# Kernel tuning notes

Hardware: AMD Instinct MI355X
Metric: run time of the kernel (lower is better)

The kernel has to match this reference:

```python
import jax, jax.numpy as jnp
import numpy as np

NUM_HEADS = 8
EPS = 1e-6


def setup_inputs() -> dict:
    key = jax.random.key(0)
    k1, k2, k3 = jax.random.split(key, 3)
    B, N, C = 4, 256, 512
    x = jax.random.normal(k1, (B, N, C), dtype=jnp.float32)
    w_qkv = jax.random.normal(k2, (3 * C, C), dtype=jnp.float32) * (C ** -0.5)
    w_proj = jax.random.normal(k3, (C, C), dtype=jnp.float32) * (C ** -0.5)
    b_proj = jnp.zeros((C,), dtype=jnp.float32)
    paramR = jnp.ones((1,), dtype=jnp.float32)
    return {"x": x, "w_qkv": w_qkv, "w_proj": w_proj, "b_proj": b_proj, "paramR": paramR}


def _fourier_attention(x, w_qkv, w_proj, b_proj, paramR):
    B, N, C = x.shape
    H = NUM_HEADS
    Dh = C // H
    # qkv projection (no bias), split into per-head q,k,v: (B,H,N,Dh)
    qkv = jnp.einsum('bnc,kc->bnk', x, w_qkv).reshape(B, N, 3, H, Dh)
    q = qkv[:, :, 0].transpose(0, 2, 1, 3)
    k = qkv[:, :, 1].transpose(0, 2, 1, 3)
    v = qkv[:, :, 2].transpose(0, 2, 1, 3)
    R = paramR[0]
    # Generalized Fourier integral kernel: prod_d sin(R*(q_d - k_d))/(q_d - k_d)
    diff = q[:, :, :, None, :] - k[:, :, None, :, :]  # (B,H,Nq,Nk,Dh)
    near0 = jnp.abs(diff) < 1e-8
    safe = jnp.where(near0, jnp.float32(1.0), diff)
    s = jnp.where(near0, R, jnp.sin(R * safe) / safe)
    score = jnp.prod(s, axis=-1)  # (B,H,Nq,Nk)
    a4 = score ** 4
    attn = a4 / (jnp.sum(a4, axis=-1, keepdims=True) + EPS)  # normalize over keys
    out = jnp.einsum('bhqk,bhkd->bhqd', attn, v)
    out = out.transpose(0, 2, 1, 3).reshape(B, N, C)
    return jnp.einsum('bnc,oc->bno', out, w_proj) + b_proj


def reference(x, w_qkv, w_proj, b_proj, paramR):
    return _fourier_attention(x, w_qkv, w_proj, b_proj, paramR)
```

## Files before the change

kernel.cpp:

```cpp
#include <hip/hip_runtime.h>
#include <math.h>

#define BB 4
#define NN 256
#define CC 512
#define HH 8
#define DH 64

typedef __attribute__((ext_vector_type(8))) short bf16x8;
typedef __attribute__((ext_vector_type(4))) float f32x4;

__device__ inline unsigned short f2bf(float f) {
  unsigned u = __float_as_uint(f);
  u += 0x7FFFu + ((u >> 16) & 1u);
  return (unsigned short)(u >> 16);
}
__device__ inline float bf2f(unsigned short s) {
  return __uint_as_float((unsigned)s << 16);
}

__global__ __launch_bounds__(256) void cvt_hilo3(
    const float* __restrict__ in0, unsigned short* __restrict__ h0,
    unsigned short* __restrict__ l0, const float* __restrict__ in1,
    unsigned short* __restrict__ h1, unsigned short* __restrict__ l1,
    const float* __restrict__ in2, unsigned short* __restrict__ h2,
    unsigned short* __restrict__ l2) {
  int b = blockIdx.x;
  const float* in;
  unsigned short *h, *l;
  if (b < 512) {
    in = in0; h = h0; l = l0;
  } else if (b < 1280) {
    in = in1; h = h1; l = l1; b -= 512;
  } else {
    in = in2; h = h2; l = l2; b -= 1280;
  }
  int i = (b * 256 + threadIdx.x) * 4;
  float4 f = *(const float4*)(in + i);
  float fa[4] = {f.x, f.y, f.z, f.w};
  ushort4 hv, lv;
  unsigned short* hp = (unsigned short*)&hv;
  unsigned short* lp = (unsigned short*)&lv;
#pragma unroll
  for (int j = 0; j < 4; j++) {
    unsigned short hb = f2bf(fa[j]);
    hp[j] = hb;
    lp[j] = f2bf(fa[j] - bf2f(hb));
  }
  *(ushort4*)(h + i) = hv;
  *(ushort4*)(l + i) = lv;
}

template <bool BIAS>
__global__ __launch_bounds__(256, 2) void gemm_mfma(
    const unsigned short* __restrict__ Ah, const unsigned short* __restrict__ Al,
    const unsigned short* __restrict__ Bh, const unsigned short* __restrict__ Bl,
    const float* __restrict__ bias, float* __restrict__ C, int M, int N,
    int K) {
  __shared__ unsigned short sAh[64][72], sAl[64][72];
  __shared__ unsigned short sBh[64][72], sBl[64][72];
  const int t = threadIdx.x;
  const int lane = t & 63;
  const int w = t >> 6;
  const int bm = blockIdx.y * 64;
  const int bn = blockIdx.x * 64;
  const int wr = (w >> 1) * 32;
  const int wc = (w & 1) * 32;
  const int quad = lane >> 4;
  const int l16 = lane & 15;

  const int r0 = t >> 3;
  const int r1 = r0 + 32;
  const int c8 = (t & 7) * 8;

  const size_t a0 = (size_t)(bm + r0) * K + c8;
  const size_t a1 = (size_t)(bm + r1) * K + c8;
  const size_t b0 = (size_t)(bn + r0) * K + c8;
  const size_t b1 = (size_t)(bn + r1) * K + c8;

  f32x4 acc[2][2];
#pragma unroll
  for (int i = 0; i < 2; i++)
#pragma unroll
    for (int j = 0; j < 2; j++) {
      acc[i][j][0] = 0.f;
      acc[i][j][1] = 0.f;
      acc[i][j][2] = 0.f;
      acc[i][j][3] = 0.f;
    }

  uint4 pa0, pa1, pa2, pa3, pb0, pb1, pb2, pb3;
#define GLOADS(K0)                          \
  pa0 = *(const uint4*)(Ah + a0 + (K0));    \
  pa1 = *(const uint4*)(Ah + a1 + (K0));    \
  pa2 = *(const uint4*)(Al + a0 + (K0));    \
  pa3 = *(const uint4*)(Al + a1 + (K0));    \
  pb0 = *(const uint4*)(Bh + b0 + (K0));    \
  pb1 = *(const uint4*)(Bh + b1 + (K0));    \
  pb2 = *(const uint4*)(Bl + b0 + (K0));    \
  pb3 = *(const uint4*)(Bl + b1 + (K0));

  GLOADS(0)

  for (int k0 = 0; k0 < K; k0 += 64) {
    __syncthreads();
    *(uint4*)&sAh[r0][c8] = pa0;
    *(uint4*)&sAh[r1][c8] = pa1;
    *(uint4*)&sAl[r0][c8] = pa2;
    *(uint4*)&sAl[r1][c8] = pa3;
    *(uint4*)&sBh[r0][c8] = pb0;
    *(uint4*)&sBh[r1][c8] = pb1;
    *(uint4*)&sBl[r0][c8] = pb2;
    *(uint4*)&sBl[r1][c8] = pb3;
    __syncthreads();
    if (k0 + 64 < K) {
      GLOADS(k0 + 64)
    }
#pragma unroll
    for (int kk = 0; kk < 2; kk++) {
      const int kc = kk * 32 + quad * 8;
      bf16x8 ah[2], al[2], bh[2], bl[2];
#pragma unroll
      for (int i = 0; i < 2; i++) {
        ah[i] = *(const bf16x8*)&sAh[wr + i * 16 + l16][kc];
        al[i] = *(const bf16x8*)&sAl[wr + i * 16 + l16][kc];
        bh[i] = *(const bf16x8*)&sBh[wc + i * 16 + l16][kc];
        bl[i] = *(const bf16x8*)&sBl[wc + i * 16 + l16][kc];
      }
#pragma unroll
      for (int i = 0; i < 2; i++)
#pragma unroll
        for (int j = 0; j < 2; j++) {
          acc[i][j] = __builtin_amdgcn_mfma_f32_16x16x32_bf16(
              ah[i], bh[j], acc[i][j], 0, 0, 0);
          acc[i][j] = __builtin_amdgcn_mfma_f32_16x16x32_bf16(
              ah[i], bl[j], acc[i][j], 0, 0, 0);
          acc[i][j] = __builtin_amdgcn_mfma_f32_16x16x32_bf16(
              al[i], bh[j], acc[i][j], 0, 0, 0);
        }
    }
  }
#undef GLOADS

#pragma unroll
  for (int i = 0; i < 2; i++)
#pragma unroll
    for (int j = 0; j < 2; j++) {
      int n = bn + wc + j * 16 + l16;
      float bv = BIAS ? bias[n] : 0.f;
#pragma unroll
      for (int r = 0; r < 4; r++) {
        int m = bm + wr + i * 16 + quad * 4 + r;
        C[(size_t)m * N + n] = acc[i][j][r] + bv;
      }
    }
}

__global__ __launch_bounds__(512, 4) void fourier_attn(
    const float* __restrict__ qkv, const float* __restrict__ paramR,
    unsigned short* __restrict__ aoh, unsigned short* __restrict__ aol) {
  __shared__ float Kt[64][68];
  __shared__ float VtT[64][68];
  __shared__ float Qs[16][DH];
  __shared__ float A4[8][64][2];

  const int t = threadIdx.x;
  const int lane = t & 63;
  const int wv = t >> 6;
  const int qc = blockIdx.x;
  const int h = blockIdx.y;
  const int b = blockIdx.z;
  const float R = paramR[0];
  const float cR = R * 0.15915494309189535f;

  const float* base = qkv + (size_t)b * NN * (3 * CC) + h * DH;

  if (t < 256) {
    int r = t >> 4;
    int c4 = (t & 15) << 2;
    *(float4*)&Qs[r][c4] =
        *(const float4*)(base + (size_t)(qc * 16 + r) * (3 * CC) + c4);
  }

  const int qi0 = wv * 2, qi1 = wv * 2 + 1;
  float Sp[2] = {0.f, 0.f};
  float acc[2] = {0.f, 0.f};

  float4 pk[2], pv[2];
#define LOADT(JT)                                                   \
  _Pragma("unroll") for (int u0 = 0; u0 < 2; u0++) {                \
    int u = t + 512 * u0;                                           \
    int r_ = u >> 4;                                                \
    int c4_ = (u & 15) << 2;                                        \
    const float* row_ = base + (size_t)((JT) * 64 + r_) * (3 * CC); \
    pk[u0] = *(const float4*)(row_ + CC + c4_);                     \
    pv[u0] = *(const float4*)(row_ + 2 * CC + c4_);                 \
  }

  LOADT(0)

  for (int jt = 0; jt < 4; jt++) {
    __syncthreads();
#pragma unroll
    for (int u0 = 0; u0 < 2; u0++) {
      int u = t + 512 * u0;
      int r = u >> 4;
      int c4 = (u & 15) << 2;
      *(float4*)&Kt[r][c4] = pk[u0];
      int rs = r ^ c4;
      float4 vv = pv[u0];
      VtT[c4 + 0][rs] = vv.x;
      VtT[c4 + 1][rs] = vv.y;
      VtT[c4 + 2][rs] = vv.z;
      VtT[c4 + 3][rs] = vv.w;
    }
    __syncthreads();
    if (jt < 3) {
      LOADT(jt + 1)
    }

    float nm[2][2] = {{1.f, 1.f}, {1.f, 1.f}};
    float dn[2][2] = {{1.f, 1.f}, {1.f, 1.f}};
#pragma unroll
    for (int d4 = 0; d4 < 16; d4++) {
      const int p = d4 & 1;
      float4 k4 = *(const float4*)&Kt[lane][4 * d4];
      float4 qa = *(const float4*)&Qs[qi0][4 * d4];
      float4 qb = *(const float4*)&Qs[qi1][4 * d4];
      float ka[4] = {k4.x, k4.y, k4.z, k4.w};
      float q0a[4] = {qa.x, qa.y, qa.z, qa.w};
      float q1a[4] = {qb.x, qb.y, qb.z, qb.w};
#pragma unroll
      for (int j = 0; j < 4; j++) {
        float d0 = q0a[j] - ka[j] + 1e-30f;
        float d1 = q1a[j] - ka[j] + 1e-30f;
        nm[0][p] *= __builtin_amdgcn_sinf(cR * d0);
        dn[0][p] *= d0;
        nm[1][p] *= __builtin_amdgcn_sinf(cR * d1);
        dn[1][p] *= d1;
      }
    }
#pragma unroll
    for (int q = 0; q < 2; q++) {
      float sc = (nm[q][0] * nm[q][1]) / (dn[q][0] * dn[q][1]);
      float s2 = sc * sc;
      float a4 = s2 * s2;
      Sp[q] += a4;
      A4[wv][lane][q] = a4;
    }

#pragma unroll
    for (int j4 = 0; j4 < 16; j4++) {
      float4 v4 = *(const float4*)&VtT[lane][(4 * j4) ^ (lane & 60)];
      float4 a01 = *(const float4*)&A4[wv][4 * j4 + 0][0];
      float4 a23 = *(const float4*)&A4[wv][4 * j4 + 2][0];
      acc[0] = fmaf(a01.x, v4.x, acc[0]);
      acc[1] = fmaf(a01.y, v4.x, acc[1]);
      acc[0] = fmaf(a01.z, v4.y, acc[0]);
      acc[1] = fmaf(a01.w, v4.y, acc[1]);
      acc[0] = fmaf(a23.x, v4.z, acc[0]);
      acc[1] = fmaf(a23.y, v4.z, acc[1]);
      acc[0] = fmaf(a23.z, v4.w, acc[0]);
      acc[1] = fmaf(a23.w, v4.w, acc[1]);
    }
  }
#undef LOADT

#pragma unroll
  for (int q = 0; q < 2; q++) {
    float s = Sp[q];
#pragma unroll
    for (int off = 32; off > 0; off >>= 1) s += __shfl_xor(s, off, 64);
    float o = acc[q] / (s + 1e-6f);
    int n = qc * 16 + wv * 2 + q;
    size_t idx = (size_t)(b * NN + n) * CC + h * DH + lane;
    unsigned short oh = f2bf(o);
    aoh[idx] = oh;
    aol[idx] = f2bf(o - bf2f(oh));
  }
}

extern "C" void kernel_launch(void* const* d_in, const int* in_sizes, int n_in,
                              void* d_out, int out_size, void* d_ws,
                              size_t ws_size, hipStream_t stream) {
  const float* x = (const float*)d_in[0];
  const float* w_qkv = (const float*)d_in[1];
  const float* w_proj = (const float*)d_in[2];
  const float* b_proj = (const float*)d_in[3];
  const float* paramR = (const float*)d_in[4];
  float* outp = (float*)d_out;

  const int nX = BB * NN * CC;
  const int nWq = 3 * CC * CC;
  const int nWp = CC * CC;

  unsigned short* xh = (unsigned short*)d_ws;
  unsigned short* xl = xh + nX;
  unsigned short* wqh = xl + nX;
  unsigned short* wql = wqh + nWq;
  unsigned short* wph = wql + nWq;
  unsigned short* wpl = wph + nWp;
  unsigned short* aoh = wpl + nWp;
  unsigned short* aol = aoh + nX;
  float* qkv_ws = (float*)(aol + nX);

  cvt_hilo3<<<1536, 256, 0, stream>>>(x, xh, xl, w_qkv, wqh, wql, w_proj, wph,
                                      wpl);

  gemm_mfma<false><<<dim3(3 * CC / 64, BB * NN / 64), 256, 0, stream>>>(
      xh, xl, wqh, wql, nullptr, qkv_ws, BB * NN, 3 * CC, CC);

  fourier_attn<<<dim3(NN / 16, HH, BB), 512, 0, stream>>>(qkv_ws, paramR, aoh,
                                                          aol);

  gemm_mfma<true><<<dim3(CC / 64, BB * NN / 64), 256, 0, stream>>>(
      aoh, aol, wph, wpl, b_proj, outp, BB * NN, CC, CC);
}
```

Before: 123.0 us.

## Use MFMA for attention PV product and double-buffer GEMM shared tiles

The scalar FMA loop for attention weights times V becomes split-bf16 (hi/lo) MFMA operations. The weights are staged in shared memory as bf16 hi/lo pairs, and the 8 waves split the key range into two halves that are reduced at the end. The GEMM kernel gains double-buffered LDS tiles, which removes one barrier per K step. The sine/product loop is also rewritten with 2-wide float vectors to encourage packed math. The cost is an extra barrier per key tile, the split-bf16 conversion overhead, and more LDS use in the GEMM.

```diff
diff --git a/kernel.cpp b/kernel.cpp
--- a/kernel.cpp
+++ b/kernel.cpp
@@ -9,6 +9,7 @@
 
 typedef __attribute__((ext_vector_type(8))) short bf16x8;
 typedef __attribute__((ext_vector_type(4))) float f32x4;
+typedef __attribute__((ext_vector_type(2))) float f32x2;
 
 __device__ inline unsigned short f2bf(float f) {
   unsigned u = __float_as_uint(f);
@@ -57,8 +58,8 @@
     const unsigned short* __restrict__ Bh, const unsigned short* __restrict__ Bl,
     const float* __restrict__ bias, float* __restrict__ C, int M, int N,
     int K) {
-  __shared__ unsigned short sAh[64][72], sAl[64][72];
-  __shared__ unsigned short sBh[64][72], sBl[64][72];
+  __shared__ unsigned short sAh[2][64][72], sAl[2][64][72];
+  __shared__ unsigned short sBh[2][64][72], sBl[2][64][72];
   const int t = threadIdx.x;
   const int lane = t & 63;
   const int w = t >> 6;
@@ -90,42 +91,43 @@
     }
 
   uint4 pa0, pa1, pa2, pa3, pb0, pb1, pb2, pb3;
-#define GLOADS(K0)                          \
-  pa0 = *(const uint4*)(Ah + a0 + (K0));    \
-  pa1 = *(const uint4*)(Ah + a1 + (K0));    \
-  pa2 = *(const uint4*)(Al + a0 + (K0));    \
-  pa3 = *(const uint4*)(Al + a1 + (K0));    \
-  pb0 = *(const uint4*)(Bh + b0 + (K0));    \
-  pb1 = *(const uint4*)(Bh + b1 + (K0));    \
-  pb2 = *(const uint4*)(Bl + b0 + (K0));    \
+#define GLOADS(K0)                       \
+  pa0 = *(const uint4*)(Ah + a0 + (K0)); \
+  pa1 = *(const uint4*)(Ah + a1 + (K0)); \
+  pa2 = *(const uint4*)(Al + a0 + (K0)); \
+  pa3 = *(const uint4*)(Al + a1 + (K0)); \
+  pb0 = *(const uint4*)(Bh + b0 + (K0)); \
+  pb1 = *(const uint4*)(Bh + b1 + (K0)); \
+  pb2 = *(const uint4*)(Bl + b0 + (K0)); \
   pb3 = *(const uint4*)(Bl + b1 + (K0));
 
+#define STORE(P)                  \
+  *(uint4*)&sAh[P][r0][c8] = pa0; \
+  *(uint4*)&sAh[P][r1][c8] = pa1; \
+  *(uint4*)&sAl[P][r0][c8] = pa2; \
+  *(uint4*)&sAl[P][r1][c8] = pa3; \
+  *(uint4*)&sBh[P][r0][c8] = pb0; \
+  *(uint4*)&sBh[P][r1][c8] = pb1; \
+  *(uint4*)&sBl[P][r0][c8] = pb2; \
+  *(uint4*)&sBl[P][r1][c8] = pb3;
+
   GLOADS(0)
-
+  STORE(0)
+  __syncthreads();
+  GLOADS(64)
+
+  int p = 0;
   for (int k0 = 0; k0 < K; k0 += 64) {
-    __syncthreads();
-    *(uint4*)&sAh[r0][c8] = pa0;
-    *(uint4*)&sAh[r1][c8] = pa1;
-    *(uint4*)&sAl[r0][c8] = pa2;
-    *(uint4*)&sAl[r1][c8] = pa3;
-    *(uint4*)&sBh[r0][c8] = pb0;
-    *(uint4*)&sBh[r1][c8] = pb1;
-    *(uint4*)&sBl[r0][c8] = pb2;
-    *(uint4*)&sBl[r1][c8] = pb3;
-    __syncthreads();
-    if (k0 + 64 < K) {
-      GLOADS(k0 + 64)
-    }
 #pragma unroll
     for (int kk = 0; kk < 2; kk++) {
       const int kc = kk * 32 + quad * 8;
       bf16x8 ah[2], al[2], bh[2], bl[2];
 #pragma unroll
       for (int i = 0; i < 2; i++) {
-        ah[i] = *(const bf16x8*)&sAh[wr + i * 16 + l16][kc];
-        al[i] = *(const bf16x8*)&sAl[wr + i * 16 + l16][kc];
-        bh[i] = *(const bf16x8*)&sBh[wc + i * 16 + l16][kc];
-        bl[i] = *(const bf16x8*)&sBl[wc + i * 16 + l16][kc];
+        ah[i] = *(const bf16x8*)&sAh[p][wr + i * 16 + l16][kc];
+        al[i] = *(const bf16x8*)&sAl[p][wr + i * 16 + l16][kc];
+        bh[i] = *(const bf16x8*)&sBh[p][wc + i * 16 + l16][kc];
+        bl[i] = *(const bf16x8*)&sBl[p][wc + i * 16 + l16][kc];
       }
 #pragma unroll
       for (int i = 0; i < 2; i++)
@@ -139,8 +141,17 @@
               al[i], bh[j], acc[i][j], 0, 0, 0);
         }
     }
+    if (k0 + 64 < K) {
+      STORE(p ^ 1)
+      if (k0 + 128 < K) {
+        GLOADS(k0 + 128)
+      }
+    }
+    __syncthreads();
+    p ^= 1;
   }
 #undef GLOADS
+#undef STORE
 
 #pragma unroll
   for (int i = 0; i < 2; i++)
@@ -160,13 +171,18 @@
     const float* __restrict__ qkv, const float* __restrict__ paramR,
     unsigned short* __restrict__ aoh, unsigned short* __restrict__ aol) {
   __shared__ float Kt[64][68];
-  __shared__ float VtT[64][68];
-  __shared__ float Qs[16][DH];
-  __shared__ float A4[8][64][2];
+  __shared__ float Vs[64][68];
+  __shared__ float Qs[16][64];
+  __shared__ unsigned short Pah[16][72];
+  __shared__ unsigned short Pal[16][72];
+  __shared__ float Sden[16];
+  __shared__ f32x4 Red[4][64];
 
   const int t = threadIdx.x;
   const int lane = t & 63;
   const int wv = t >> 6;
+  const int quad = lane >> 4;
+  const int l16 = lane & 15;
   const int qc = blockIdx.x;
   const int h = blockIdx.y;
   const int b = blockIdx.z;
@@ -184,7 +200,12 @@
 
   const int qi0 = wv * 2, qi1 = wv * 2 + 1;
   float Sp[2] = {0.f, 0.f};
-  float acc[2] = {0.f, 0.f};
+  f32x4 oacc;
+  oacc[0] = 0.f; oacc[1] = 0.f; oacc[2] = 0.f; oacc[3] = 0.f;
+
+  const int nc = wv & 3;
+  const int g2 = wv >> 2;
+  const int kb = g2 * 32 + quad * 8;
 
   float4 pk[2], pv[2];
 #define LOADT(JT)                                                   \
@@ -199,6 +220,9 @@
 
   LOADT(0)
 
+  const f32x2 eps2 = {1e-30f, 1e-30f};
+  const f32x2 cR2 = {cR, cR};
+
   for (int jt = 0; jt < 4; jt++) {
     __syncthreads();
 #pragma unroll
@@ -207,61 +231,79 @@
       int r = u >> 4;
       int c4 = (u & 15) << 2;
       *(float4*)&Kt[r][c4] = pk[u0];
-      int rs = r ^ c4;
-      float4 vv = pv[u0];
-      VtT[c4 + 0][rs] = vv.x;
-      VtT[c4 + 1][rs] = vv.y;
-      VtT[c4 + 2][rs] = vv.z;
-      VtT[c4 + 3][rs] = vv.w;
+      *(float4*)&Vs[r][c4] = pv[u0];
     }
     __syncthreads();
     if (jt < 3) {
       LOADT(jt + 1)
     }
 
-    float nm[2][2] = {{1.f, 1.f}, {1.f, 1.f}};
-    float dn[2][2] = {{1.f, 1.f}, {1.f, 1.f}};
+    f32x2 nmA0 = {1.f, 1.f}, nmB0 = {1.f, 1.f};
+    f32x2 nmA1 = {1.f, 1.f}, nmB1 = {1.f, 1.f};
+    f32x2 dnA0 = {1.f, 1.f}, dnB0 = {1.f, 1.f};
+    f32x2 dnA1 = {1.f, 1.f}, dnB1 = {1.f, 1.f};
 #pragma unroll
     for (int d4 = 0; d4 < 16; d4++) {
-      const int p = d4 & 1;
       float4 k4 = *(const float4*)&Kt[lane][4 * d4];
       float4 qa = *(const float4*)&Qs[qi0][4 * d4];
       float4 qb = *(const float4*)&Qs[qi1][4 * d4];
-      float ka[4] = {k4.x, k4.y, k4.z, k4.w};
-      float q0a[4] = {qa.x, qa.y, qa.z, qa.w};
-      float q1a[4] = {qb.x, qb.y, qb.z, qb.w};
-#pragma unroll
-      for (int j = 0; j < 4; j++) {
-        float d0 = q0a[j] - ka[j] + 1e-30f;
-        float d1 = q1a[j] - ka[j] + 1e-30f;
-        nm[0][p] *= __builtin_amdgcn_sinf(cR * d0);
-        dn[0][p] *= d0;
-        nm[1][p] *= __builtin_amdgcn_sinf(cR * d1);
-        dn[1][p] *= d1;
+      f32x2 kA = {k4.x, k4.y};
+      f32x2 kB = {k4.z, k4.w};
+      f32x2 dA0 = ((f32x2){qa.x, qa.y} - kA) + eps2;
+      f32x2 dB0 = ((f32x2){qa.z, qa.w} - kB) + eps2;
+      f32x2 dA1 = ((f32x2){qb.x, qb.y} - kA) + eps2;
+      f32x2 dB1 = ((f32x2){qb.z, qb.w} - kB) + eps2;
+      f32x2 gA0 = cR2 * dA0, gB0 = cR2 * dB0;
+      f32x2 gA1 = cR2 * dA1, gB1 = cR2 * dB1;
+      f32x2 sA0, sB0, sA1, sB1;
+      sA0.x = __builtin_amdgcn_sinf(gA0.x);
+      sA0.y = __builtin_amdgcn_sinf(gA0.y);
+      sB0.x = __builtin_amdgcn_sinf(gB0.x);
+      sB0.y = __builtin_amdgcn_sinf(gB0.y);
+      sA1.x = __builtin_amdgcn_sinf(gA1.x);
+      sA1.y = __builtin_amdgcn_sinf(gA1.y);
+      sB1.x = __builtin_amdgcn_sinf(gB1.x);
+      sB1.y = __builtin_amdgcn_sinf(gB1.y);
+      nmA0 *= sA0;
+      nmB0 *= sB0;
+      nmA1 *= sA1;
+      nmB1 *= sB1;
+      dnA0 *= dA0;
+      dnB0 *= dB0;
+      dnA1 *= dA1;
+      dnB1 *= dB1;
+    }
+    {
+      f32x2 n0 = nmA0 * nmB0, d0 = dnA0 * dnB0;
+      f32x2 n1 = nmA1 * nmB1, d1 = dnA1 * dnB1;
+      float sc0 = (n0.x * n0.y) / (d0.x * d0.y);
+      float sc1 = (n1.x * n1.y) / (d1.x * d1.y);
+      float t0 = sc0 * sc0, t1 = sc1 * sc1;
+      float a40 = t0 * t0, a41 = t1 * t1;
+      Sp[0] += a40;
+      Sp[1] += a41;
+      unsigned short h0 = f2bf(a40), h1 = f2bf(a41);
+      Pah[qi0][lane] = h0;
+      Pal[qi0][lane] = f2bf(a40 - bf2f(h0));
+      Pah[qi1][lane] = h1;
+      Pal[qi1][lane] = f2bf(a41 - bf2f(h1));
+    }
+    __syncthreads();
+
+    {
+      bf16x8 pah = *(const bf16x8*)&Pah[l16][kb];
+      bf16x8 pal = *(const bf16x8*)&Pal[l16][kb];
+      bf16x8 vh, vl;
+#pragma unroll
+      for (int j = 0; j < 8; j++) {
+        float f = Vs[kb + j][nc * 16 + l16];
+        unsigned short hb = f2bf(f);
+        vh[j] = (short)hb;
+        vl[j] = (short)f2bf(f - bf2f(hb));
       }
-    }
-#pragma unroll
-    for (int q = 0; q < 2; q++) {
-      float sc = (nm[q][0] * nm[q][1]) / (dn[q][0] * dn[q][1]);
-      float s2 = sc * sc;
-      float a4 = s2 * s2;
-      Sp[q] += a4;
-      A4[wv][lane][q] = a4;
-    }
-
-#pragma unroll
-    for (int j4 = 0; j4 < 16; j4++) {
-      float4 v4 = *(const float4*)&VtT[lane][(4 * j4) ^ (lane & 60)];
-      float4 a01 = *(const float4*)&A4[wv][4 * j4 + 0][0];
-      float4 a23 = *(const float4*)&A4[wv][4 * j4 + 2][0];
-      acc[0] = fmaf(a01.x, v4.x, acc[0]);
-      acc[1] = fmaf(a01.y, v4.x, acc[1]);
-      acc[0] = fmaf(a01.z, v4.y, acc[0]);
-      acc[1] = fmaf(a01.w, v4.y, acc[1]);
-      acc[0] = fmaf(a23.x, v4.z, acc[0]);
-      acc[1] = fmaf(a23.y, v4.z, acc[1]);
-      acc[0] = fmaf(a23.z, v4.w, acc[0]);
-      acc[1] = fmaf(a23.w, v4.w, acc[1]);
+      oacc = __builtin_amdgcn_mfma_f32_16x16x32_bf16(pah, vh, oacc, 0, 0, 0);
+      oacc = __builtin_amdgcn_mfma_f32_16x16x32_bf16(pah, vl, oacc, 0, 0, 0);
+      oacc = __builtin_amdgcn_mfma_f32_16x16x32_bf16(pal, vh, oacc, 0, 0, 0);
     }
   }
 #undef LOADT
@@ -271,12 +313,23 @@
     float s = Sp[q];
 #pragma unroll
     for (int off = 32; off > 0; off >>= 1) s += __shfl_xor(s, off, 64);
-    float o = acc[q] / (s + 1e-6f);
-    int n = qc * 16 + wv * 2 + q;
-    size_t idx = (size_t)(b * NN + n) * CC + h * DH + lane;
-    unsigned short oh = f2bf(o);
-    aoh[idx] = oh;
-    aol[idx] = f2bf(o - bf2f(oh));
+    if (lane == 0) Sden[qi0 + q] = s;
+  }
+  if (wv >= 4) Red[wv - 4][lane] = oacc;
+  __syncthreads();
+  if (wv < 4) {
+    f32x4 part = Red[wv][lane];
+#pragma unroll
+    for (int r = 0; r < 4; r++) {
+      int q = quad * 4 + r;
+      float s = Sden[q];
+      float o = (oacc[r] + part[r]) / (s + 1e-6f);
+      int n = qc * 16 + q;
+      size_t idx = (size_t)(b * NN + n) * CC + h * DH + nc * 16 + l16;
+      unsigned short oh = f2bf(o);
+      aoh[idx] = oh;
+      aol[idx] = f2bf(o - bf2f(oh));
+    }
   }
 }
 
```

Measured after the change: 123.3 us. Within noise of the previous version (+0.3%).
